# Kernel optimization log

Hardware: AMD Instinct MI355X
Metric: run time of the kernel (lower is better)

## Reference

```python
import jax, jax.numpy as jnp
import numpy as np

N = 10000        # nodes
E = 640000       # edges (before self-loops)
D_IN = 128
D_OUT = 128
NEG_SLOPE = 0.2  # PyG GATConv default


def setup_inputs() -> dict:
    key = jax.random.key(0)
    k1, k2, k3, k4, k5 = jax.random.split(key, 5)
    x = jax.random.normal(k1, (N, D_IN), dtype=jnp.float32)
    edge_index = jax.random.randint(k2, (2, E), 0, N, dtype=jnp.int64)
    # learned params of GATConv(in, out, heads=1)
    W = jax.random.normal(k3, (D_IN, D_OUT), dtype=jnp.float32) / np.sqrt(D_IN).astype(np.float32)
    att_src = jax.random.normal(k4, (D_OUT,), dtype=jnp.float32) * 0.1
    att_dst = jax.random.normal(k5, (D_OUT,), dtype=jnp.float32) * 0.1
    bias = jnp.zeros((D_OUT,), dtype=jnp.float32)
    return {"x": x, "W": W, "att_src": att_src, "att_dst": att_dst,
            "bias": bias, "edge_index": edge_index}


def reference(x, W, att_src, att_dst, bias, edge_index):
    # PyG GATConv default: add self-loops
    loop = jnp.arange(N, dtype=edge_index.dtype)
    src = jnp.concatenate([edge_index[0], loop])  # [E+N]
    dst = jnp.concatenate([edge_index[1], loop])  # [E+N]

    h = x @ W                          # [N, D_OUT]
    a_s = h @ att_src                  # [N] per-node source logit
    a_d = h @ att_dst                  # [N] per-node dest logit

    # per-edge attention logits, LeakyReLU(0.2)
    e = jax.nn.leaky_relu(a_s[src] + a_d[dst], negative_slope=NEG_SLOPE)  # [E+N]

    # segment softmax over incoming edges of each destination node
    m = jax.ops.segment_max(e, dst, num_segments=N)       # [N]
    m = jax.lax.stop_gradient(m)
    ex = jnp.exp(e - m[dst])
    denom = jax.ops.segment_sum(ex, dst, num_segments=N)  # [N]
    alpha = ex / denom[dst]                                # [E+N]

    # weighted scatter-aggregate of transformed source features
    msgs = alpha[:, None] * h[src]                         # [E+N, D_OUT]
    out = jax.ops.segment_sum(msgs, dst, num_segments=N)   # [N, D_OUT]
    return out + bias
```

## Files before the change

### kernel.cpp

```cpp
#include <hip/hip_runtime.h>
#include <hip/hip_bf16.h>

#define N_NODES 10000
#define E_EDGES 640000
#define D_IN 128
#define D_OUT 128
#define NEG_SLOPE 0.2f

#define BSH 3
#define NBIN 1250
#define NFB 256
#define FCHUNK 2500
#define RSTRIDE 1280
#define DCAP 160

typedef unsigned short ushort_t;
typedef unsigned int uint_t;
typedef __attribute__((ext_vector_type(8))) short short8;
typedef __attribute__((ext_vector_type(4))) float v4f;

static __device__ __forceinline__ float bf2f(uint_t u) {
  return __uint_as_float(u << 16);
}
static __device__ __forceinline__ ushort_t f2bf(float f) {
  unsigned int x = __float_as_uint(f);
  return (ushort_t)((x + 0x7fffu + ((x >> 16) & 1u)) >> 16);
}

union SmemU {
  struct {
    ushort_t Wt[128 * 132];
    float asum[16], dsum[16];
  } g;
  struct {
    int hist[NBIN];
    int cur[NBIN];
    int scanA[256], scanB[256];
    int sortedL[FCHUNK];
  } f;
};

__global__ __launch_bounds__(256) void gat_main(
    const float* __restrict__ x, const float* __restrict__ W,
    const float* __restrict__ att_src, const float* __restrict__ att_dst,
    const int* __restrict__ src, const int* __restrict__ dst,
    ushort_t* __restrict__ hb, float* __restrict__ a_s, float* __restrict__ a_d,
    int* __restrict__ sortedg, uint_t* __restrict__ runinfo) {
  __shared__ SmemU sm;
  const int t = threadIdx.x;

  if (blockIdx.x < NFB) {
    const int b = blockIdx.x;
    const int4* s4 = reinterpret_cast<const int4*>(src + b * FCHUNK);
    const int4* d4 = reinterpret_cast<const int4*>(dst + b * FCHUNK);
    for (int i = t; i < NBIN; i += 256) sm.f.hist[i] = 0;

    int4 sv[3], dv[3];
    #pragma unroll
    for (int it = 0; it < 3; ++it) {
      const int i = t + it * 256;
      if (i < FCHUNK / 4) { sv[it] = s4[i]; dv[it] = d4[i]; }
    }
    __syncthreads();

    #pragma unroll
    for (int it = 0; it < 3; ++it) {
      const int i = t + it * 256;
      if (i < FCHUNK / 4) {
        atomicAdd(&sm.f.hist[dv[it].x >> BSH], 1);
        atomicAdd(&sm.f.hist[dv[it].y >> BSH], 1);
        atomicAdd(&sm.f.hist[dv[it].z >> BSH], 1);
        atomicAdd(&sm.f.hist[dv[it].w >> BSH], 1);
      }
    }
    __syncthreads();

    int localv[5];
    int ssum = 0;
    #pragma unroll
    for (int j = 0; j < 5; ++j) {
      const int bb = 5 * t + j;
      const int v = (bb < NBIN) ? sm.f.hist[bb] : 0;
      localv[j] = ssum;
      ssum += v;
    }
    sm.f.scanA[t] = ssum;
    __syncthreads();
    int* pa = sm.f.scanA;
    int* pb = sm.f.scanB;
    for (int off = 1; off < 256; off <<= 1) {
      int s = pa[t];
      if (t >= off) s += pa[t - off];
      pb[t] = s;
      __syncthreads();
      int* tmp = pa; pa = pb; pb = tmp;
    }
    const int excl = pa[t] - ssum;
    #pragma unroll
    for (int j = 0; j < 5; ++j) {
      const int bb = 5 * t + j;
      if (bb < NBIN) sm.f.cur[bb] = excl + localv[j];
    }
    __syncthreads();

    #pragma unroll
    for (int it = 0; it < 3; ++it) {
      const int i = t + it * 256;
      if (i < FCHUNK / 4) {
        #pragma unroll
        for (int j = 0; j < 4; ++j) {
          const int s = (j == 0) ? sv[it].x : (j == 1) ? sv[it].y
                      : (j == 2) ? sv[it].z : sv[it].w;
          const int d = (j == 0) ? dv[it].x : (j == 1) ? dv[it].y
                      : (j == 2) ? dv[it].z : dv[it].w;
          const int rel = atomicAdd(&sm.f.cur[d >> BSH], 1);
          sm.f.sortedL[rel] = s | ((d & 7) << 14);
        }
      }
    }
    __syncthreads();

    const int4* sl4 = reinterpret_cast<const int4*>(sm.f.sortedL);
    int4* sg4 = reinterpret_cast<int4*>(sortedg + (size_t)b * FCHUNK);
    for (int i = t; i < FCHUNK / 4; i += 256) sg4[i] = sl4[i];
    for (int k = t; k < NBIN; k += 256)
      runinfo[b * RSTRIDE + k] =
          (uint_t)(sm.f.cur[k] - sm.f.hist[k]) | ((uint_t)sm.f.hist[k] << 16);

  } else {
    const int l = t & 63, w = t >> 6;
    const int ln16 = l & 15, kg = l >> 4;
    const int r0 = (blockIdx.x - NFB) * 16;
    const int k0base = kg * 8;

    {
      const int c = t & 127;
      const int khb = (t >> 7) * 4;
      for (int kb = khb; kb < 128; kb += 8) {
        const float f0 = W[(kb + 0) * D_OUT + c];
        const float f1 = W[(kb + 1) * D_OUT + c];
        const float f2 = W[(kb + 2) * D_OUT + c];
        const float f3 = W[(kb + 3) * D_OUT + c];
        const uint_t p0 = (uint_t)f2bf(f0) | ((uint_t)f2bf(f1) << 16);
        const uint_t p1 = (uint_t)f2bf(f2) | ((uint_t)f2bf(f3) << 16);
        *reinterpret_cast<uint_t*>(&sm.g.Wt[c * 132 + kb]) = p0;
        *reinterpret_cast<uint_t*>(&sm.g.Wt[c * 132 + kb + 2]) = p1;
      }
    }
    if (t < 16) { sm.g.asum[t] = 0.f; sm.g.dsum[t] = 0.f; }

    short8 afrag[4];
    #pragma unroll
    for (int kt = 0; kt < 4; ++kt) {
      const int k0 = kt * 32 + k0base;
      const float4* xp = reinterpret_cast<const float4*>(
          x + (size_t)(r0 + ln16) * D_IN + k0);
      const float4 x0 = xp[0], x1 = xp[1];
      short8 af;
      af[0] = (short)f2bf(x0.x); af[1] = (short)f2bf(x0.y);
      af[2] = (short)f2bf(x0.z); af[3] = (short)f2bf(x0.w);
      af[4] = (short)f2bf(x1.x); af[5] = (short)f2bf(x1.y);
      af[6] = (short)f2bf(x1.z); af[7] = (short)f2bf(x1.w);
      afrag[kt] = af;
    }
    __syncthreads();

    const int cb0 = w * 32, cb1 = w * 32 + 16;
    v4f acc0 = {0.f, 0.f, 0.f, 0.f};
    v4f acc1 = {0.f, 0.f, 0.f, 0.f};
    #pragma unroll
    for (int kt = 0; kt < 4; ++kt) {
      const int k0 = kt * 32 + k0base;
      union { uint2 q[2]; short8 s; } b0, b1;
      b0.q[0] = *reinterpret_cast<const uint2*>(&sm.g.Wt[(cb0 + ln16) * 132 + k0]);
      b0.q[1] = *reinterpret_cast<const uint2*>(&sm.g.Wt[(cb0 + ln16) * 132 + k0 + 4]);
      b1.q[0] = *reinterpret_cast<const uint2*>(&sm.g.Wt[(cb1 + ln16) * 132 + k0]);
      b1.q[1] = *reinterpret_cast<const uint2*>(&sm.g.Wt[(cb1 + ln16) * 132 + k0 + 4]);
      acc0 = __builtin_amdgcn_mfma_f32_16x16x32_bf16(afrag[kt], b0.s, acc0, 0, 0, 0);
      acc1 = __builtin_amdgcn_mfma_f32_16x16x32_bf16(afrag[kt], b1.s, acc1, 0, 0, 0);
    }

    const float ats0 = att_src[cb0 + ln16], ats1 = att_src[cb1 + ln16];
    const float atd0 = att_dst[cb0 + ln16], atd1 = att_dst[cb1 + ln16];
    #pragma unroll
    for (int reg = 0; reg < 4; ++reg) {
      const int R = kg * 4 + reg;
      hb[(size_t)(r0 + R) * D_OUT + cb0 + ln16] = f2bf(acc0[reg]);
      hb[(size_t)(r0 + R) * D_OUT + cb1 + ln16] = f2bf(acc1[reg]);
      float ps = acc0[reg] * ats0 + acc1[reg] * ats1;
      float pd = acc0[reg] * atd0 + acc1[reg] * atd1;
      #pragma unroll
      for (int off = 8; off >= 1; off >>= 1) {
        ps += __shfl_xor(ps, off, 16);
        pd += __shfl_xor(pd, off, 16);
      }
      if (ln16 == 0) {
        atomicAdd(&sm.g.asum[R], ps);
        atomicAdd(&sm.g.dsum[R], pd);
      }
    }
    __syncthreads();
    if (t < 16) { a_s[r0 + t] = sm.g.asum[t]; a_d[r0 + t] = sm.g.dsum[t]; }
  }
}

__global__ __launch_bounds__(256, 6) void gat_aggregate(
    const ushort_t* __restrict__ hb, const int* __restrict__ sortedg,
    const uint_t* __restrict__ runinfo, const float* __restrict__ a_s,
    const float* __restrict__ a_d, const float* __restrict__ bias,
    float* __restrict__ out) {
  __shared__ int2 seg[8 * DCAP];
  __shared__ float adl[8];
  __shared__ int curs[8];
  const int B = blockIdx.x, t = threadIdx.x;
  const int xcd = B & 7, idx = B >> 3;
  const int j = (xcd < 2 ? xcd * 157 : 314 + (xcd - 2) * 156) + idx;
  const int hw = t >> 5, ln = t & 31;

  if (t < 8) { curs[t] = 0; adl[t] = a_d[j * 8 + t]; }
  const uint_t riU = runinfo[t * RSTRIDE + j];
  __syncthreads();

  {
    const int rbase = t * FCHUNK + (int)(riU & 0xffffu);
    const int rcnt = (int)(riU >> 16);
    int r = 0;
    while (r < rcnt) {
      const int nb = min(rcnt - r, 8);
      int rec[8];
      float av[8];
      #pragma unroll
      for (int u = 0; u < 8; ++u)
        if (u < nb) rec[u] = sortedg[rbase + r + u];
      #pragma unroll
      for (int u = 0; u < 8; ++u)
        if (u < nb) av[u] = a_s[rec[u] & 16383];
      #pragma unroll
      for (int u = 0; u < 8; ++u)
        if (u < nb) {
          const int dl = (rec[u] >> 14) & 7;
          float lv = av[u] + adl[dl];
          lv = fmaxf(lv, NEG_SLOPE * lv);
          const int pos = atomicAdd(&curs[dl], 1);
          if (pos < DCAP)
            seg[dl * DCAP + pos] =
                make_int2(rec[u] & 16383, __float_as_int(__expf(lv)));
        }
      r += nb;
    }
  }
  __syncthreads();

  if (t < 8) {
    const int c = min(curs[t], DCAP);
    const int cp = min((c + 7) & ~7, DCAP);
    for (int p = c; p < cp; ++p)
      seg[t * DCAP + p] = make_int2(j * 8 + t, 0);
    curs[t] = cp;
  }
  __syncthreads();

  const int d = j * 8 + hw;
  const int cp = curs[hw];
  const int2* sj = &seg[hw * DCAP];
  const char* hbase = (const char*)hb + ln * 8;
  float ax = 0.f, ay = 0.f, az = 0.f, aw = 0.f, sex = 0.f;
  for (int i = 0; i + 8 <= cp; i += 8) {
    int2 p[8];
    *reinterpret_cast<int4*>(&p[0]) = *reinterpret_cast<const int4*>(&sj[i]);
    *reinterpret_cast<int4*>(&p[2]) = *reinterpret_cast<const int4*>(&sj[i + 2]);
    *reinterpret_cast<int4*>(&p[4]) = *reinterpret_cast<const int4*>(&sj[i + 4]);
    *reinterpret_cast<int4*>(&p[6]) = *reinterpret_cast<const int4*>(&sj[i + 6]);
    ushort4 hv[8];
    #pragma unroll
    for (int u = 0; u < 8; ++u)
      hv[u] = *reinterpret_cast<const ushort4*>(
          hbase + (size_t)(p[u].x) * 256);
    #pragma unroll
    for (int u = 0; u < 8; ++u) {
      const float e = __int_as_float(p[u].y);
      ax += e * bf2f(hv[u].x); ay += e * bf2f(hv[u].y);
      az += e * bf2f(hv[u].z); aw += e * bf2f(hv[u].w);
      sex += e;
    }
  }
  float lv = a_s[d] + adl[hw];
  lv = lv > 0.f ? lv : NEG_SLOPE * lv;
  const float es = __expf(lv);
  const ushort4 hs = *reinterpret_cast<const ushort4*>(hbase + (size_t)d * 256);
  ax += es * bf2f(hs.x); ay += es * bf2f(hs.y);
  az += es * bf2f(hs.z); aw += es * bf2f(hs.w);
  sex += es;

  const float4 bv = reinterpret_cast<const float4*>(bias)[ln];
  const float inv = 1.f / sex;
  v4f ov;
  ov[0] = ax * inv + bv.x; ov[1] = ay * inv + bv.y;
  ov[2] = az * inv + bv.z; ov[3] = aw * inv + bv.w;
  __builtin_nontemporal_store(ov, reinterpret_cast<v4f*>(out) +
                                      (size_t)d * 32 + ln);
}

extern "C" void kernel_launch(void* const* d_in, const int* in_sizes, int n_in,
                              void* d_out, int out_size, void* d_ws, size_t ws_size,
                              hipStream_t stream) {
  const float* x       = (const float*)d_in[0];
  const float* W       = (const float*)d_in[1];
  const float* att_src = (const float*)d_in[2];
  const float* att_dst = (const float*)d_in[3];
  const float* bias    = (const float*)d_in[4];
  const int*   ei      = (const int*)d_in[5];
  const int* src = ei;
  const int* dst = ei + E_EDGES;
  float* out = (float*)d_out;

  char* ws = (char*)d_ws;
  ushort_t* hb      = (ushort_t*)(ws);
  float*    a_s     = (float*)(ws + 2560000);
  float*    a_d     = (float*)(ws + 2600000);
  int*      sortedg = (int*)  (ws + 2640000);
  uint_t*   runinfo = (uint_t*)(ws + 5200000);

  gat_main<<<NFB + 625, 256, 0, stream>>>(x, W, att_src, att_dst, src, dst,
                                          hb, a_s, a_d, sortedg, runinfo);

  gat_aggregate<<<NBIN, 256, 0, stream>>>(hb, sortedg, runinfo,
                                          a_s, a_d, bias, out);
}
```

Baseline: 36.81 us.

## Replace shared atomic bucket cursors with block prefix-scan slot assignment

The aggregate kernel's LDS atomicAdd cursor allocation is replaced by packed per-thread byte counters for the 8 destinations, a 256-wide Hillis-Steele scan, and deterministic in-thread offset computation. Record loads are hoisted into registers up front. The gather loop also prefetches the next 8 segment entries from LDS while the current feature loads are in flight. This removes atomic contention and makes edge ordering deterministic, but adds 8 scan steps each ending in a barrier, plus O(n^2) position counting inside a thread.

```diff
diff --git a/kernel.cpp b/kernel.cpp
--- a/kernel.cpp
+++ b/kernel.cpp
@@ -212,47 +212,126 @@
   __shared__ int2 seg[8 * DCAP];
   __shared__ float adl[8];
   __shared__ int curs[8];
+  __shared__ uint2 scA[256], scB[256];
   const int B = blockIdx.x, t = threadIdx.x;
   const int xcd = B & 7, idx = B >> 3;
   const int j = (xcd < 2 ? xcd * 157 : 314 + (xcd - 2) * 156) + idx;
   const int hw = t >> 5, ln = t & 31;
 
-  if (t < 8) { curs[t] = 0; adl[t] = a_d[j * 8 + t]; }
+  if (t < 8) adl[t] = a_d[j * 8 + t];
   const uint_t riU = runinfo[t * RSTRIDE + j];
+  const int rcnt = (int)(riU >> 16);
+  const int rbase = t * FCHUNK + (int)(riU & 0xffffu);
+
+  int recA[8], recB[8];
+  #pragma unroll
+  for (int u = 0; u < 8; ++u) if (u < rcnt) recA[u] = sortedg[rbase + u];
+  #pragma unroll
+  for (int u = 0; u < 8; ++u) if (u + 8 < rcnt) recB[u] = sortedg[rbase + 8 + u];
+
+  uint_t pcx = 0, pcy = 0;
+  #pragma unroll
+  for (int u = 0; u < 8; ++u)
+    if (u < rcnt) {
+      const int dl = (recA[u] >> 14) & 7;
+      const uint_t inc = 1u << ((dl & 3) * 8);
+      if (dl < 4) pcx += inc; else pcy += inc;
+    }
+  #pragma unroll
+  for (int u = 0; u < 8; ++u)
+    if (u + 8 < rcnt) {
+      const int dl = (recB[u] >> 14) & 7;
+      const uint_t inc = 1u << ((dl & 3) * 8);
+      if (dl < 4) pcx += inc; else pcy += inc;
+    }
+  for (int r = 16; r < rcnt; ++r) {
+    const int dl = (sortedg[rbase + r] >> 14) & 7;
+    const uint_t inc = 1u << ((dl & 3) * 8);
+    if (dl < 4) pcx += inc; else pcy += inc;
+  }
+
+  scA[t] = make_uint2(pcx, pcy);
   __syncthreads();
+  uint2* pa = scA;
+  uint2* pb = scB;
+  for (int off = 1; off < 256; off <<= 1) {
+    uint2 s = pa[t];
+    if (t >= off) { const uint2 q = pa[t - off]; s.x += q.x; s.y += q.y; }
+    pb[t] = s;
+    __syncthreads();
+    uint2* tmp = pa; pa = pb; pb = tmp;
+  }
+  const uint2 incl = pa[t];
+  const uint_t ex_x = incl.x - pcx, ex_y = incl.y - pcy;
+  if (t == 255) {
+    #pragma unroll
+    for (int dl = 0; dl < 8; ++dl) {
+      const uint_t w = dl < 4 ? incl.x : incl.y;
+      curs[dl] = min((int)((w >> ((dl & 3) * 8)) & 0xffu), DCAP);
+    }
+  }
 
   {
-    const int rbase = t * FCHUNK + (int)(riU & 0xffffu);
-    const int rcnt = (int)(riU >> 16);
-    int r = 0;
-    while (r < rcnt) {
-      const int nb = min(rcnt - r, 8);
-      int rec[8];
-      float av[8];
+    float av[8], bv[8];
+    #pragma unroll
+    for (int u = 0; u < 8; ++u) if (u < rcnt) av[u] = a_s[recA[u] & 16383];
+    #pragma unroll
+    for (int u = 0; u < 8; ++u) if (u + 8 < rcnt) bv[u] = a_s[recB[u] & 16383];
+    #pragma unroll
+    for (int u = 0; u < 8; ++u)
+      if (u < rcnt) {
+        const int dl = (recA[u] >> 14) & 7;
+        const uint_t w = dl < 4 ? ex_x : ex_y;
+        int pos = (int)((w >> ((dl & 3) * 8)) & 0xffu);
+        #pragma unroll
+        for (int v = 0; v < 8; ++v)
+          if (v < u) pos += (((recA[v] >> 14) & 7) == dl);
+        float lv = av[u] + adl[dl];
+        lv = fmaxf(lv, NEG_SLOPE * lv);
+        if (pos < DCAP)
+          seg[dl * DCAP + pos] =
+              make_int2(recA[u] & 16383, __float_as_int(__expf(lv)));
+      }
+    #pragma unroll
+    for (int u = 0; u < 8; ++u)
+      if (u + 8 < rcnt) {
+        const int dl = (recB[u] >> 14) & 7;
+        const uint_t w = dl < 4 ? ex_x : ex_y;
+        int pos = (int)((w >> ((dl & 3) * 8)) & 0xffu);
+        #pragma unroll
+        for (int v = 0; v < 8; ++v) {
+          if (v < rcnt) pos += (((recA[v] >> 14) & 7) == dl);
+          if (v < u)    pos += (((recB[v] >> 14) & 7) == dl);
+        }
+        float lv = bv[u] + adl[dl];
+        lv = fmaxf(lv, NEG_SLOPE * lv);
+        if (pos < DCAP)
+          seg[dl * DCAP + pos] =
+              make_int2(recB[u] & 16383, __float_as_int(__expf(lv)));
+      }
+    for (int r = 16; r < rcnt; ++r) {
+      const int rec = sortedg[rbase + r];
+      const int dl = (rec >> 14) & 7;
+      const uint_t w = dl < 4 ? ex_x : ex_y;
+      int pos = (int)((w >> ((dl & 3) * 8)) & 0xffu);
       #pragma unroll
-      for (int u = 0; u < 8; ++u)
-        if (u < nb) rec[u] = sortedg[rbase + r + u];
-      #pragma unroll
-      for (int u = 0; u < 8; ++u)
-        if (u < nb) av[u] = a_s[rec[u] & 16383];
-      #pragma unroll
-      for (int u = 0; u < 8; ++u)
-        if (u < nb) {
-          const int dl = (rec[u] >> 14) & 7;
-          float lv = av[u] + adl[dl];
-          lv = fmaxf(lv, NEG_SLOPE * lv);
-          const int pos = atomicAdd(&curs[dl], 1);
-          if (pos < DCAP)
-            seg[dl * DCAP + pos] =
-                make_int2(rec[u] & 16383, __float_as_int(__expf(lv)));
-        }
-      r += nb;
+      for (int v = 0; v < 8; ++v) {
+        if (v < rcnt)     pos += (((recA[v] >> 14) & 7) == dl);
+        if (v + 8 < rcnt) pos += (((recB[v] >> 14) & 7) == dl);
+      }
+      for (int v = 16; v < r; ++v)
+        pos += (((sortedg[rbase + v] >> 14) & 7) == dl);
+      float lv = a_s[rec & 16383] + adl[dl];
+      lv = fmaxf(lv, NEG_SLOPE * lv);
+      if (pos < DCAP)
+        seg[dl * DCAP + pos] =
+            make_int2(rec & 16383, __float_as_int(__expf(lv)));
     }
   }
   __syncthreads();
 
   if (t < 8) {
-    const int c = min(curs[t], DCAP);
+    const int c = curs[t];
     const int cp = min((c + 7) & ~7, DCAP);
     for (int p = c; p < cp; ++p)
       seg[t * DCAP + p] = make_int2(j * 8 + t, 0);
@@ -265,23 +344,38 @@
   const int2* sj = &seg[hw * DCAP];
   const char* hbase = (const char*)hb + ln * 8;
   float ax = 0.f, ay = 0.f, az = 0.f, aw = 0.f, sex = 0.f;
-  for (int i = 0; i + 8 <= cp; i += 8) {
-    int2 p[8];
-    *reinterpret_cast<int4*>(&p[0]) = *reinterpret_cast<const int4*>(&sj[i]);
-    *reinterpret_cast<int4*>(&p[2]) = *reinterpret_cast<const int4*>(&sj[i + 2]);
-    *reinterpret_cast<int4*>(&p[4]) = *reinterpret_cast<const int4*>(&sj[i + 4]);
-    *reinterpret_cast<int4*>(&p[6]) = *reinterpret_cast<const int4*>(&sj[i + 6]);
+  int2 p[8];
+  if (cp > 0) {
+    *reinterpret_cast<int4*>(&p[0]) = *reinterpret_cast<const int4*>(&sj[0]);
+    *reinterpret_cast<int4*>(&p[2]) = *reinterpret_cast<const int4*>(&sj[2]);
+    *reinterpret_cast<int4*>(&p[4]) = *reinterpret_cast<const int4*>(&sj[4]);
+    *reinterpret_cast<int4*>(&p[6]) = *reinterpret_cast<const int4*>(&sj[6]);
+  }
+  for (int i = 0; i < cp; i += 8) {
     ushort4 hv[8];
     #pragma unroll
     for (int u = 0; u < 8; ++u)
       hv[u] = *reinterpret_cast<const ushort4*>(
           hbase + (size_t)(p[u].x) * 256);
+    int2 pn[8];
+    const bool more = (i + 8) < cp;
+    if (more) {
+      const int2* sn = &sj[i + 8];
+      *reinterpret_cast<int4*>(&pn[0]) = *reinterpret_cast<const int4*>(&sn[0]);
+      *reinterpret_cast<int4*>(&pn[2]) = *reinterpret_cast<const int4*>(&sn[2]);
+      *reinterpret_cast<int4*>(&pn[4]) = *reinterpret_cast<const int4*>(&sn[4]);
+      *reinterpret_cast<int4*>(&pn[6]) = *reinterpret_cast<const int4*>(&sn[6]);
+    }
     #pragma unroll
     for (int u = 0; u < 8; ++u) {
       const float e = __int_as_float(p[u].y);
       ax += e * bf2f(hv[u].x); ay += e * bf2f(hv[u].y);
       az += e * bf2f(hv[u].z); aw += e * bf2f(hv[u].w);
       sex += e;
+    }
+    if (more) {
+      #pragma unroll
+      for (int u = 0; u < 8; ++u) p[u] = pn[u];
     }
   }
   float lv = a_s[d] + adl[hw];
@@ -292,11 +386,11 @@
   az += es * bf2f(hs.z); aw += es * bf2f(hs.w);
   sex += es;
 
-  const float4 bv = reinterpret_cast<const float4*>(bias)[ln];
+  const float4 bvv = reinterpret_cast<const float4*>(bias)[ln];
   const float inv = 1.f / sex;
   v4f ov;
-  ov[0] = ax * inv + bv.x; ov[1] = ay * inv + bv.y;
-  ov[2] = az * inv + bv.z; ov[3] = aw * inv + bv.w;
+  ov[0] = ax * inv + bvv.x; ov[1] = ay * inv + bvv.y;
+  ov[2] = az * inv + bvv.z; ov[3] = aw * inv + bvv.w;
   __builtin_nontemporal_store(ov, reinterpret_cast<v4f*>(out) +
                                       (size_t)d * 32 + ln);
 }
```

New measurement: 37.26 us. No clear change (+1.2%).
